# Kernel optimization log

Measured on AMD Instinct MI355X. Metric: run time of the kernel, lower is better.

The kernel has to match this reference:

```python
import jax, jax.numpy as jnp
import numpy as np

E, H, O = 64, 128, 16  # enc_hidden_dim, dec_hidden_dim, dec_output_dim (proj_size)
B, N, FUT = 64, 1000, 12


def _lstm_proj_cell(x, h, c, W_ih, W_hh, b_ih, b_hh, W_hr):
    # PyTorch gate order: input, forget, cell(g), output
    gates = x @ W_ih.T + h @ W_hh.T + (b_ih + b_hh)
    i, f, g, o = jnp.split(gates, 4, axis=-1)
    c_new = jax.nn.sigmoid(f) * c + jax.nn.sigmoid(i) * jnp.tanh(g)
    h_full = jax.nn.sigmoid(o) * jnp.tanh(c_new)
    h_new = h_full @ W_hr.T  # proj_size projection
    return h_new, c_new


def setup_inputs() -> dict:
    key = jax.random.key(0)
    ks = jax.random.split(key, 20)
    sc = 0.1
    inp = {
        "enc_outputs": jax.random.normal(ks[0], (B, 1, N, E), jnp.float32),
        "mean": jax.random.normal(ks[1], (B, FUT, N, O), jnp.float32),
        "s": jax.random.normal(ks[2], (1, O), jnp.float32),
        "h_0": jax.random.normal(ks[3], (2, O), jnp.float32),
        "c_0": jax.random.normal(ks[4], (2, H), jnp.float32),
        "W_ih_l0": sc * jax.random.normal(ks[5], (4 * H, E + O), jnp.float32),
        "W_hh_l0": sc * jax.random.normal(ks[6], (4 * H, O), jnp.float32),
        "b_ih_l0": sc * jax.random.normal(ks[7], (4 * H,), jnp.float32),
        "b_hh_l0": sc * jax.random.normal(ks[8], (4 * H,), jnp.float32),
        "W_hr_l0": sc * jax.random.normal(ks[9], (O, H), jnp.float32),
        "W_ih_l1": sc * jax.random.normal(ks[10], (4 * H, O), jnp.float32),
        "W_hh_l1": sc * jax.random.normal(ks[11], (4 * H, O), jnp.float32),
        "b_ih_l1": sc * jax.random.normal(ks[12], (4 * H,), jnp.float32),
        "b_hh_l1": sc * jax.random.normal(ks[13], (4 * H,), jnp.float32),
        "W_hr_l1": sc * jax.random.normal(ks[14], (O, H), jnp.float32),
        "future": FUT,
    }
    # forget-gate bias = 1.0 as in reset_bias()
    for nme in ("b_ih_l0", "b_hh_l0", "b_ih_l1", "b_hh_l1"):
        inp[nme] = inp[nme].at[H:2 * H].set(1.0)
    return inp


def _forward(enc_outputs, mean, s, h_0, c_0,
             W_ih_l0, W_hh_l0, b_ih_l0, b_hh_l0, W_hr_l0,
             W_ih_l1, W_hh_l1, b_ih_l1, b_hh_l1, W_hr_l1, future):
    b, _, n_nodes, _ = enc_outputs.shape
    enc = enc_outputs[:, 0]            # [B, N, E]
    node_mean = jnp.mean(mean, axis=1)  # [B, N, O]
    # state is carried across nodes AND timesteps: one chain of N*future steps
    node_idx = jnp.arange(n_nodes * future) // future

    last0 = jnp.broadcast_to(s[0], (b, s.shape[1]))
    h1_0 = jnp.broadcast_to(h_0[0], (b, h_0.shape[1]))
    h2_0 = jnp.broadcast_to(h_0[1], (b, h_0.shape[1]))
    c1_0 = jnp.broadcast_to(c_0[0], (b, c_0.shape[1]))
    c2_0 = jnp.broadcast_to(c_0[1], (b, c_0.shape[1]))

    def step(carry, n):
        last, h1, c1, h2, c2 = carry
        enc_t = jnp.take(enc, n, axis=1)        # [B, E]
        nm_t = jnp.take(node_mean, n, axis=1)   # [B, O]
        loop = last + nm_t                      # TFRate forced to 0.0 in source
        x = jnp.concatenate([enc_t, loop], axis=-1)
        h1, c1 = _lstm_proj_cell(x, h1, c1, W_ih_l0, W_hh_l0, b_ih_l0, b_hh_l0, W_hr_l0)
        h2, c2 = _lstm_proj_cell(h1, h2, c2, W_ih_l1, W_hh_l1, b_ih_l1, b_hh_l1, W_hr_l1)
        return (h2, h1, c1, h2, c2), h2 + nm_t

    _, outs = jax.lax.scan(step, (last0, h1_0, c1_0, h2_0, c2_0), node_idx)
    # outs: [N*future, B, O] -> [B, future, N, O]
    outs = outs.reshape(n_nodes, future, b, -1).transpose(2, 1, 0, 3)
    return outs


def reference(enc_outputs, mean, s, h_0, c_0,
              W_ih_l0, W_hh_l0, b_ih_l0, b_hh_l0, W_hr_l0,
              W_ih_l1, W_hh_l1, b_ih_l1, b_hh_l1, W_hr_l1, future):
    return _forward(enc_outputs, mean, s, h_0, c_0,
                    W_ih_l0, W_hh_l0, b_ih_l0, b_hh_l0, W_hr_l0,
                    W_ih_l1, W_hh_l1, b_ih_l1, b_hh_l1, W_hr_l1, future)
```

## Files before the change

### kernel.cpp

```cpp
#include <hip/hip_runtime.h>

#define BB 64
#define NN 1000
#define FF 12
#define EE 64
#define HH 128
#define OO 16

__device__ __forceinline__ float rcp_(float x){ return __builtin_amdgcn_rcpf(x); }
__device__ __forceinline__ float sigm_(float x){ return rcp_(1.0f + __expf(-x)); }
__device__ __forceinline__ float tanh_(float x){ return 1.0f - 2.0f*rcp_(__expf(2.0f*x) + 1.0f); }

__device__ __forceinline__ float4 fma4(float4 a, float4 x, float4 w){
    a.x += x.x*w.x; a.y += x.y*w.y; a.z += x.z*w.z; a.w += x.w*w.w; return a;
}
__device__ __forceinline__ float hsum4(float4 a){ return (a.x+a.y)+(a.z+a.w); }

__global__ __launch_bounds__(256, 1)
void decoder_kernel(const float* __restrict__ enc,
                    const float* __restrict__ mean,
                    const float* __restrict__ sv,
                    const float* __restrict__ h0,
                    const float* __restrict__ c0,
                    const float* __restrict__ Wih0,
                    const float* __restrict__ Whh0,
                    const float* __restrict__ bih0,
                    const float* __restrict__ bhh0,
                    const float* __restrict__ Whr0,
                    const float* __restrict__ Wih1,
                    const float* __restrict__ Whh1,
                    const float* __restrict__ bih1,
                    const float* __restrict__ bhh1,
                    const float* __restrict__ Whr1,
                    float* __restrict__ out)
{
    const int t = threadIdx.x;
    const int b = blockIdx.x;

    const int u  = t >> 1;
    const int m  = t & 1;
    const int rA = m*HH + u;
    const int rB = rA + 2*HH;

    const int lane = t & 63;
    const int j16  = lane >> 2;
    const int q    = lane & 3;

    __shared__ __align__(16) float s_last[OO];
    __shared__ __align__(16) float s_h1[OO];
    __shared__ __align__(16) float s_h2[OO];
    __shared__ __align__(16) float s_enc[EE];
    __shared__ __align__(16) float s_nm[OO];
    __shared__ __align__(16) float s_hf[4*36];
    __shared__ __align__(16) float s_out[FF*OO];

    float4 wAl[4], wBl[4], wAh[4], wBh[4];
    float4 w1Ai[4], w1Bi[4], w1Ah[4], w1Bh[4];
    #pragma unroll
    for (int k=0;k<4;k++){
        wAl[k]  = *(const float4*)&Wih0[(size_t)rA*(EE+OO) + EE + 4*k];
        wBl[k]  = *(const float4*)&Wih0[(size_t)rB*(EE+OO) + EE + 4*k];
        wAh[k]  = *(const float4*)&Whh0[rA*OO + 4*k];
        wBh[k]  = *(const float4*)&Whh0[rB*OO + 4*k];
        w1Ai[k] = *(const float4*)&Wih1[rA*OO + 4*k];
        w1Bi[k] = *(const float4*)&Wih1[rB*OO + 4*k];
        w1Ah[k] = *(const float4*)&Whh1[rA*OO + 4*k];
        w1Bh[k] = *(const float4*)&Whh1[rB*OO + 4*k];
    }
    const float b0A = bih0[rA] + bhh0[rA];
    const float b0B = bih0[rB] + bhh0[rB];
    const float b1A = bih1[rA] + bhh1[rA];
    const float b1B = bih1[rB] + bhh1[rB];

    float4 wp0[8], wp1[8];
    #pragma unroll
    for (int i=0;i<8;i++){
        wp0[i] = *(const float4*)&Whr0[j16*HH + q*32 + 4*i];
        wp1[i] = *(const float4*)&Whr1[j16*HH + q*32 + 4*i];
    }

    float c1u = c0[u];
    float c2u = c0[HH + u];

    if (t < OO){
        s_last[t] = sv[t];
        s_h1[t]   = h0[t];
        s_h2[t]   = h0[OO + t];
    }

    const float* encB  = enc  + (size_t)b * NN * EE;
    const float* meanB = mean + (size_t)b * FF * NN * OO;
    float*       outB  = out  + (size_t)b * FF * NN * OO;

    const float4* wrowA = (const float4*)(Wih0 + (size_t)rA*(EE+OO));
    const float4* wrowB = (const float4*)(Wih0 + (size_t)rB*(EE+OO));

    float4 pf_enc = make_float4(0,0,0,0);
    float  pf_nm[FF];
    if (t < 16){
        pf_enc = ((const float4*)encB)[t];
    } else if (t < 32){
        const int j = t - 16;
        #pragma unroll
        for (int ff=0; ff<FF; ++ff) pf_nm[ff] = meanB[(size_t)(ff*NN)*OO + j];
    }

    for (int n = 0; n < NN; ++n){
        if (t < 16){
            ((float4*)s_enc)[t] = pf_enc;
        } else if (t < 32){
            float a0 = pf_nm[0]+pf_nm[4], a1 = pf_nm[1]+pf_nm[5];
            float a2 = pf_nm[2]+pf_nm[6], a3 = pf_nm[3]+pf_nm[7];
            a0 += pf_nm[8]; a1 += pf_nm[9]; a2 += pf_nm[10]; a3 += pf_nm[11];
            s_nm[t-16] = ((a0+a1)+(a2+a3)) * (1.0f/12.0f);
        }
        __syncthreads();

        const int n1 = (n+1 < NN) ? (n+1) : n;
        if (t < 16){
            pf_enc = ((const float4*)encB)[n1*16 + t];
        } else if (t < 32){
            const int j = t - 16;
            #pragma unroll
            for (int ff=0; ff<FF; ++ff) pf_nm[ff] = meanB[(size_t)(ff*NN + n1)*OO + j];
        }

        float preA, preB;
        {
            float4 sa = make_float4(b0A, 0.f, 0.f, 0.f);
            float4 sb = make_float4(b0B, 0.f, 0.f, 0.f);
            #pragma unroll
            for (int k=0;k<16;k++){
                const float4 e = ((const float4*)s_enc)[k];
                sa = fma4(sa, e, wrowA[k]);
                sb = fma4(sb, e, wrowB[k]);
            }
            float4 nm4[4];
            #pragma unroll
            for (int k=0;k<4;k++) nm4[k] = ((const float4*)s_nm)[k];
            #pragma unroll
            for (int k=0;k<4;k++){ sa = fma4(sa, nm4[k], wAl[k]); sb = fma4(sb, nm4[k], wBl[k]); }
            preA = hsum4(sa);
            preB = hsum4(sb);
        }
        const float nmj = s_nm[j16];

        #pragma unroll 1
        for (int f = 0; f < FF; ++f){
            {
                float4 L[4], H[4];
                #pragma unroll
                for (int k=0;k<4;k++){ L[k] = ((const float4*)s_last)[k]; H[k] = ((const float4*)s_h1)[k]; }
                float4 accA = make_float4(preA, 0.f, 0.f, 0.f);
                float4 accB = make_float4(preB, 0.f, 0.f, 0.f);
                #pragma unroll
                for (int k=0;k<4;k++){
                    accA = fma4(accA, L[k], wAl[k]); accA = fma4(accA, H[k], wAh[k]);
                    accB = fma4(accB, L[k], wBl[k]); accB = fma4(accB, H[k], wBh[k]);
                }
                const float aA = hsum4(accA);
                const float aB = hsum4(accB);
                const float gA = sigm_(aA);
                const float gB = (m==0) ? tanh_(aB) : sigm_(aB);
                const float sendv = (m==0) ? gA*gB : gA;
                const float recvv = __shfl_xor(sendv, 1, 64);
                const float Fv    = (m==0) ? recvv : sendv;
                const float prod  = (m==0) ? sendv : recvv;
                c1u = Fv*c1u + prod;
                if (m) s_hf[u + ((u>>5)<<2)] = gB * tanh_(c1u);
            }
            __syncthreads();

            {
                float4 acc = make_float4(0.f,0.f,0.f,0.f);
                #pragma unroll
                for (int i=0;i<8;i++){
                    const float4 h = *(const float4*)&s_hf[q*36 + 4*i];
                    acc = fma4(acc, h, wp0[i]);
                }
                float p = hsum4(acc);
                p += __shfl_xor(p, 1, 64);
                p += __shfl_xor(p, 2, 64);
                if (t < 64 && q == 0) s_h1[j16] = p;
            }
            __syncthreads();

            {
                float4 X[4], H[4];
                #pragma unroll
                for (int k=0;k<4;k++){ X[k] = ((const float4*)s_h1)[k]; H[k] = ((const float4*)s_h2)[k]; }
                float4 accA = make_float4(b1A, 0.f, 0.f, 0.f);
                float4 accB = make_float4(b1B, 0.f, 0.f, 0.f);
                #pragma unroll
                for (int k=0;k<4;k++){
                    accA = fma4(accA, X[k], w1Ai[k]); accA = fma4(accA, H[k], w1Ah[k]);
                    accB = fma4(accB, X[k], w1Bi[k]); accB = fma4(accB, H[k], w1Bh[k]);
                }
                const float aA = hsum4(accA);
                const float aB = hsum4(accB);
                const float gA = sigm_(aA);
                const float gB = (m==0) ? tanh_(aB) : sigm_(aB);
                const float sendv = (m==0) ? gA*gB : gA;
                const float recvv = __shfl_xor(sendv, 1, 64);
                const float Fv    = (m==0) ? recvv : sendv;
                const float prod  = (m==0) ? sendv : recvv;
                c2u = Fv*c2u + prod;
                if (m) s_hf[u + ((u>>5)<<2)] = gB * tanh_(c2u);
            }
            __syncthreads();

            {
                float4 acc = make_float4(0.f,0.f,0.f,0.f);
                #pragma unroll
                for (int i=0;i<8;i++){
                    const float4 h = *(const float4*)&s_hf[q*36 + 4*i];
                    acc = fma4(acc, h, wp1[i]);
                }
                float p = hsum4(acc);
                p += __shfl_xor(p, 1, 64);
                p += __shfl_xor(p, 2, 64);
                if (t < 64 && q == 0){
                    s_h2[j16]   = p;
                    s_last[j16] = p;
                    s_out[f*OO + j16] = p + nmj;
                }
            }
            __syncthreads();
        }

        if (t < 48){
            const int ff = t >> 2, o4 = (t & 3) * 4;
            const float4 v = *(const float4*)&s_out[ff*OO + o4];
            *(float4*)&outB[(size_t)(ff*NN + n)*OO + o4] = v;
        }
    }
}

extern "C" void kernel_launch(void* const* d_in, const int* in_sizes, int n_in,
                              void* d_out, int out_size, void* d_ws, size_t ws_size,
                              hipStream_t stream) {
    const float* enc  = (const float*)d_in[0];
    const float* mean = (const float*)d_in[1];
    const float* sv   = (const float*)d_in[2];
    const float* h0   = (const float*)d_in[3];
    const float* c0   = (const float*)d_in[4];
    const float* Wih0 = (const float*)d_in[5];
    const float* Whh0 = (const float*)d_in[6];
    const float* bih0 = (const float*)d_in[7];
    const float* bhh0 = (const float*)d_in[8];
    const float* Whr0 = (const float*)d_in[9];
    const float* Wih1 = (const float*)d_in[10];
    const float* Whh1 = (const float*)d_in[11];
    const float* bih1 = (const float*)d_in[12];
    const float* bhh1 = (const float*)d_in[13];
    const float* Whr1 = (const float*)d_in[14];
    float* out = (float*)d_out;

    decoder_kernel<<<dim3(BB), dim3(256), 0, stream>>>(
        enc, mean, sv, h0, c0,
        Wih0, Whh0, bih0, bhh0, Whr0,
        Wih1, Whh1, bih1, bhh1, Whr1,
        out);
}
```

Measured before the change: 17.08 ms.

## Replicate the projection per wave to halve block barriers per LSTM step

Each of the four waves now computes the hidden-state projections redundantly into its own shared-memory slot. The next gate computation then reads only wave-local data, so two of the four __syncthreads per timestep can go, and layer-0 gates for the next step are folded into the same phase as layer-1's projection. The per-node enc and mean loads are no longer prefetched a node ahead; they are loaded right before the barrier, and output stores are deferred by one node. This trades extra redundant FMAs and exposed global-load latency per node for fewer block-wide barriers on the serial critical path.

```diff
diff --git a/kernel.cpp b/kernel.cpp
--- a/kernel.cpp
+++ b/kernel.cpp
@@ -34,25 +34,28 @@
                     const float* __restrict__ Whr1,
                     float* __restrict__ out)
 {
-    const int t = threadIdx.x;
-    const int b = blockIdx.x;
+    const int t  = threadIdx.x;
+    const int b  = blockIdx.x;
+    const int wv = t >> 6;
+    const int lane = t & 63;
 
     const int u  = t >> 1;
     const int m  = t & 1;
     const int rA = m*HH + u;
     const int rB = rA + 2*HH;
 
-    const int lane = t & 63;
-    const int j16  = lane >> 2;
-    const int q    = lane & 3;
-
-    __shared__ __align__(16) float s_last[OO];
-    __shared__ __align__(16) float s_h1[OO];
-    __shared__ __align__(16) float s_h2[OO];
+    const int j = lane >> 2;
+    const int q = lane & 3;
+    const int hfpad = u + ((u>>5)<<2);
+
+    __shared__ __align__(16) float s_hf1[4*36];
+    __shared__ __align__(16) float s_hf2[4*36];
+    __shared__ __align__(16) float s_hw1[4][OO];
+    __shared__ __align__(16) float s_hw2[4][OO];
     __shared__ __align__(16) float s_enc[EE];
     __shared__ __align__(16) float s_nm[OO];
-    __shared__ __align__(16) float s_hf[4*36];
     __shared__ __align__(16) float s_out[FF*OO];
+    __shared__ __align__(16) float s_bh2[OO];
 
     float4 wAl[4], wBl[4], wAh[4], wBh[4];
     float4 w1Ai[4], w1Bi[4], w1Ah[4], w1Bh[4];
@@ -75,18 +78,20 @@
     float4 wp0[8], wp1[8];
     #pragma unroll
     for (int i=0;i<8;i++){
-        wp0[i] = *(const float4*)&Whr0[j16*HH + q*32 + 4*i];
-        wp1[i] = *(const float4*)&Whr1[j16*HH + q*32 + 4*i];
+        wp0[i] = *(const float4*)&Whr0[j*HH + q*32 + 4*i];
+        wp1[i] = *(const float4*)&Whr1[j*HH + q*32 + 4*i];
     }
 
     float c1u = c0[u];
     float c2u = c0[HH + u];
 
-    if (t < OO){
-        s_last[t] = sv[t];
-        s_h1[t]   = h0[t];
-        s_h2[t]   = h0[OO + t];
-    }
+    float4 h1v[4], h2v[4];
+    #pragma unroll
+    for (int k=0;k<4;k++){
+        h1v[k] = *(const float4*)&h0[4*k];
+        h2v[k] = *(const float4*)&sv[4*k];
+    }
+    if (t < OO) s_bh2[t] = h0[OO + t];
 
     const float* encB  = enc  + (size_t)b * NN * EE;
     const float* meanB = mean + (size_t)b * FF * NN * OO;
@@ -95,144 +100,128 @@
     const float4* wrowA = (const float4*)(Wih0 + (size_t)rA*(EE+OO));
     const float4* wrowB = (const float4*)(Wih0 + (size_t)rB*(EE+OO));
 
-    float4 pf_enc = make_float4(0,0,0,0);
-    float  pf_nm[FF];
-    if (t < 16){
-        pf_enc = ((const float4*)encB)[t];
-    } else if (t < 32){
-        const int j = t - 16;
+    float preA = 0.f, preB = 0.f, nmj = 0.f;
+
+    auto gates0 = [&](){
+        float4 accA = make_float4(preA,0.f,0.f,0.f);
+        float4 accB = make_float4(preB,0.f,0.f,0.f);
         #pragma unroll
-        for (int ff=0; ff<FF; ++ff) pf_nm[ff] = meanB[(size_t)(ff*NN)*OO + j];
-    }
+        for (int k=0;k<4;k++){
+            accA = fma4(accA, h2v[k], wAl[k]); accA = fma4(accA, h1v[k], wAh[k]);
+            accB = fma4(accB, h2v[k], wBl[k]); accB = fma4(accB, h1v[k], wBh[k]);
+        }
+        const float aA = hsum4(accA), aB = hsum4(accB);
+        const float gA = sigm_(aA);
+        const float gB = (m==0) ? tanh_(aB) : sigm_(aB);
+        const float sendv = (m==0) ? gA*gB : gA;
+        const float recvv = __shfl_xor(sendv, 1, 64);
+        const float Fv    = (m==0) ? recvv : sendv;
+        const float prod  = (m==0) ? sendv : recvv;
+        c1u = Fv*c1u + prod;
+        if (m) s_hf1[hfpad] = gB * tanh_(c1u);
+    };
+    auto gates1 = [&](){
+        float4 accA = make_float4(b1A,0.f,0.f,0.f);
+        float4 accB = make_float4(b1B,0.f,0.f,0.f);
+        #pragma unroll
+        for (int k=0;k<4;k++){
+            accA = fma4(accA, h1v[k], w1Ai[k]); accA = fma4(accA, h2v[k], w1Ah[k]);
+            accB = fma4(accB, h1v[k], w1Bi[k]); accB = fma4(accB, h2v[k], w1Bh[k]);
+        }
+        const float aA = hsum4(accA), aB = hsum4(accB);
+        const float gA = sigm_(aA);
+        const float gB = (m==0) ? tanh_(aB) : sigm_(aB);
+        const float sendv = (m==0) ? gA*gB : gA;
+        const float recvv = __shfl_xor(sendv, 1, 64);
+        const float Fv    = (m==0) ? recvv : sendv;
+        const float prod  = (m==0) ? sendv : recvv;
+        c2u = Fv*c2u + prod;
+        if (m) s_hf2[hfpad] = gB * tanh_(c2u);
+    };
 
     for (int n = 0; n < NN; ++n){
+        if (n > 0 && t < 48){
+            const int ff = t >> 2, o4 = (t & 3) * 4;
+            *(float4*)&outB[(size_t)(ff*NN + (n-1))*OO + o4] =
+                *(const float4*)&s_out[ff*OO + o4];
+        }
         if (t < 16){
-            ((float4*)s_enc)[t] = pf_enc;
-        } else if (t < 32){
-            float a0 = pf_nm[0]+pf_nm[4], a1 = pf_nm[1]+pf_nm[5];
-            float a2 = pf_nm[2]+pf_nm[6], a3 = pf_nm[3]+pf_nm[7];
-            a0 += pf_nm[8]; a1 += pf_nm[9]; a2 += pf_nm[10]; a3 += pf_nm[11];
-            s_nm[t-16] = ((a0+a1)+(a2+a3)) * (1.0f/12.0f);
+            ((float4*)s_enc)[t] = ((const float4*)(encB + (size_t)n*EE))[t];
+        } else if (t >= 64 && t < 80){
+            const int jj = t - 64;
+            float a = 0.0f;
+            #pragma unroll
+            for (int ff=0; ff<FF; ++ff) a += meanB[(size_t)(ff*NN + n)*OO + jj];
+            s_nm[jj] = a * (1.0f/12.0f);
         }
         __syncthreads();
 
-        const int n1 = (n+1 < NN) ? (n+1) : n;
-        if (t < 16){
-            pf_enc = ((const float4*)encB)[n1*16 + t];
-        } else if (t < 32){
-            const int j = t - 16;
-            #pragma unroll
-            for (int ff=0; ff<FF; ++ff) pf_nm[ff] = meanB[(size_t)(ff*NN + n1)*OO + j];
-        }
-
-        float preA, preB;
         {
-            float4 sa = make_float4(b0A, 0.f, 0.f, 0.f);
-            float4 sb = make_float4(b0B, 0.f, 0.f, 0.f);
+            float4 sa = make_float4(b0A,0.f,0.f,0.f);
+            float4 sb = make_float4(b0B,0.f,0.f,0.f);
             #pragma unroll
             for (int k=0;k<16;k++){
                 const float4 e = ((const float4*)s_enc)[k];
                 sa = fma4(sa, e, wrowA[k]);
                 sb = fma4(sb, e, wrowB[k]);
             }
-            float4 nm4[4];
             #pragma unroll
-            for (int k=0;k<4;k++) nm4[k] = ((const float4*)s_nm)[k];
-            #pragma unroll
-            for (int k=0;k<4;k++){ sa = fma4(sa, nm4[k], wAl[k]); sb = fma4(sb, nm4[k], wBl[k]); }
-            preA = hsum4(sa);
-            preB = hsum4(sb);
-        }
-        const float nmj = s_nm[j16];
+            for (int k=0;k<4;k++){
+                const float4 nm4 = ((const float4*)s_nm)[k];
+                sa = fma4(sa, nm4, wAl[k]); sb = fma4(sb, nm4, wBl[k]);
+            }
+            preA = hsum4(sa); preB = hsum4(sb);
+        }
+        nmj = s_nm[j];
+
+        gates0();
+        __syncthreads();
 
         #pragma unroll 1
         for (int f = 0; f < FF; ++f){
             {
-                float4 L[4], H[4];
-                #pragma unroll
-                for (int k=0;k<4;k++){ L[k] = ((const float4*)s_last)[k]; H[k] = ((const float4*)s_h1)[k]; }
-                float4 accA = make_float4(preA, 0.f, 0.f, 0.f);
-                float4 accB = make_float4(preB, 0.f, 0.f, 0.f);
-                #pragma unroll
-                for (int k=0;k<4;k++){
-                    accA = fma4(accA, L[k], wAl[k]); accA = fma4(accA, H[k], wAh[k]);
-                    accB = fma4(accB, L[k], wBl[k]); accB = fma4(accB, H[k], wBh[k]);
-                }
-                const float aA = hsum4(accA);
-                const float aB = hsum4(accB);
-                const float gA = sigm_(aA);
-                const float gB = (m==0) ? tanh_(aB) : sigm_(aB);
-                const float sendv = (m==0) ? gA*gB : gA;
-                const float recvv = __shfl_xor(sendv, 1, 64);
-                const float Fv    = (m==0) ? recvv : sendv;
-                const float prod  = (m==0) ? sendv : recvv;
-                c1u = Fv*c1u + prod;
-                if (m) s_hf[u + ((u>>5)<<2)] = gB * tanh_(c1u);
-            }
-            __syncthreads();
-
-            {
                 float4 acc = make_float4(0.f,0.f,0.f,0.f);
                 #pragma unroll
-                for (int i=0;i<8;i++){
-                    const float4 h = *(const float4*)&s_hf[q*36 + 4*i];
-                    acc = fma4(acc, h, wp0[i]);
-                }
+                for (int i=0;i<8;i++)
+                    acc = fma4(acc, *(const float4*)&s_hf1[q*36 + 4*i], wp0[i]);
                 float p = hsum4(acc);
                 p += __shfl_xor(p, 1, 64);
                 p += __shfl_xor(p, 2, 64);
-                if (t < 64 && q == 0) s_h1[j16] = p;
-            }
-            __syncthreads();
-
-            {
-                float4 X[4], H[4];
-                #pragma unroll
-                for (int k=0;k<4;k++){ X[k] = ((const float4*)s_h1)[k]; H[k] = ((const float4*)s_h2)[k]; }
-                float4 accA = make_float4(b1A, 0.f, 0.f, 0.f);
-                float4 accB = make_float4(b1B, 0.f, 0.f, 0.f);
-                #pragma unroll
-                for (int k=0;k<4;k++){
-                    accA = fma4(accA, X[k], w1Ai[k]); accA = fma4(accA, H[k], w1Ah[k]);
-                    accB = fma4(accB, X[k], w1Bi[k]); accB = fma4(accB, H[k], w1Bh[k]);
+                if (q == 0) s_hw1[wv][j] = p;
+                if (n == 0 && f == 0){
+                    #pragma unroll
+                    for (int k=0;k<4;k++) h2v[k] = ((const float4*)s_bh2)[k];
                 }
-                const float aA = hsum4(accA);
-                const float aB = hsum4(accB);
-                const float gA = sigm_(aA);
-                const float gB = (m==0) ? tanh_(aB) : sigm_(aB);
-                const float sendv = (m==0) ? gA*gB : gA;
-                const float recvv = __shfl_xor(sendv, 1, 64);
-                const float Fv    = (m==0) ? recvv : sendv;
-                const float prod  = (m==0) ? sendv : recvv;
-                c2u = Fv*c2u + prod;
-                if (m) s_hf[u + ((u>>5)<<2)] = gB * tanh_(c2u);
+                #pragma unroll
+                for (int k=0;k<4;k++) h1v[k] = ((const float4*)&s_hw1[wv][0])[k];
+                gates1();
             }
             __syncthreads();
 
             {
                 float4 acc = make_float4(0.f,0.f,0.f,0.f);
                 #pragma unroll
-                for (int i=0;i<8;i++){
-                    const float4 h = *(const float4*)&s_hf[q*36 + 4*i];
-                    acc = fma4(acc, h, wp1[i]);
-                }
+                for (int i=0;i<8;i++)
+                    acc = fma4(acc, *(const float4*)&s_hf2[q*36 + 4*i], wp1[i]);
                 float p = hsum4(acc);
                 p += __shfl_xor(p, 1, 64);
                 p += __shfl_xor(p, 2, 64);
-                if (t < 64 && q == 0){
-                    s_h2[j16]   = p;
-                    s_last[j16] = p;
-                    s_out[f*OO + j16] = p + nmj;
+                if (q == 0){
+                    s_hw2[wv][j] = p;
+                    if (wv == 0) s_out[f*OO + j] = p + nmj;
                 }
+                #pragma unroll
+                for (int k=0;k<4;k++) h2v[k] = ((const float4*)&s_hw2[wv][0])[k];
+                if (f < FF-1) gates0();
             }
             __syncthreads();
         }
-
-        if (t < 48){
-            const int ff = t >> 2, o4 = (t & 3) * 4;
-            const float4 v = *(const float4*)&s_out[ff*OO + o4];
-            *(float4*)&outB[(size_t)(ff*NN + n)*OO + o4] = v;
-        }
+    }
+
+    if (t < 48){
+        const int ff = t >> 2, o4 = (t & 3) * 4;
+        *(float4*)&outB[(size_t)(ff*NN + (NN-1))*OO + o4] =
+            *(const float4*)&s_out[ff*OO + o4];
     }
 }
 
```

After: 18.72 ms. +9.7%, slower.
